# Optimization experiments

Measured on AMD Instinct MI355X. Metric: run time of the kernel, lower is better.

## Reference

```python
import jax, jax.numpy as jnp
import numpy as np

N = 100000   # mesh vertices
E = 600000   # directed edges
H = 128      # hidden dim
Z = 64       # latent (aggregated voxel feature) dim per block
IN = 6       # vertices(3) + vector_potential(3)
BIN = H + Z + IN  # 198, block input dim after concat
OUT = 3      # E-field components


def graph_conv(x, src, dst, Ws, Wn, b, n_nodes, act=True):
    # gather source-node features, mean-aggregate onto destination nodes
    msg = jax.ops.segment_sum(x[src], dst, num_segments=n_nodes)          # [N, F]
    deg = jax.ops.segment_sum(jnp.ones((src.shape[0], 1), x.dtype), dst,
                              num_segments=n_nodes)                        # [N, 1]
    nb = msg / jnp.maximum(deg, 1.0)
    out = x @ Ws + nb @ Wn + b
    return jax.nn.relu(out) if act else out


def setup_inputs() -> dict:
    key = jax.random.key(0)
    ks = jax.random.split(key, 12)
    s = 0.05
    vertices = jax.random.normal(ks[0], (N, 3), jnp.float32)
    vector_potential = jax.random.normal(ks[1], (N, 3), jnp.float32)
    z = jax.random.normal(ks[2], (4, N, Z), jnp.float32)
    edges = jax.random.randint(ks[3], (E, 2), 0, N, jnp.int64)
    # graph_conv_first: IN -> H
    W0s = jax.random.normal(ks[4], (IN, H), jnp.float32) * s
    W0n = jax.random.normal(ks[5], (IN, H), jnp.float32) * s
    b0 = jnp.zeros((H,), jnp.float32)
    # 4 gnn blocks: BIN -> H (stacked)
    Wbs = jax.random.normal(ks[6], (4, BIN, H), jnp.float32) * s
    Wbn = jax.random.normal(ks[7], (4, BIN, H), jnp.float32) * s
    bb = jnp.zeros((4, H), jnp.float32)
    # graph_conv_last: H -> OUT (no activation)
    Wls = jax.random.normal(ks[8], (H, OUT), jnp.float32) * s
    Wln = jax.random.normal(ks[9], (H, OUT), jnp.float32) * s
    bl = jnp.zeros((OUT,), jnp.float32)
    return {"vertices": vertices, "edges": edges,
            "vector_potential": vector_potential, "z": z,
            "W0s": W0s, "W0n": W0n, "b0": b0,
            "Wbs": Wbs, "Wbn": Wbn, "bb": bb,
            "Wls": Wls, "Wln": Wln, "bl": bl}


def reference(vertices, edges, vector_potential, z,
              W0s, W0n, b0, Wbs, Wbn, bb, Wls, Wln, bl):
    src = edges[:, 0]
    dst = edges[:, 1]
    n = vertices.shape[0]
    input_features = jnp.concatenate([vertices, vector_potential], axis=-1)  # [N, 6]
    features = graph_conv(input_features, src, dst, W0s, W0n, b0, n)          # [N, H]
    for i in range(4):  # fixed, structurally distinct blocks
        features = jnp.concatenate([features, z[i], input_features], axis=-1)  # [N, 198]
        features = graph_conv(features, src, dst, Wbs[i], Wbn[i], bb[i], n)    # [N, H]
    features = graph_conv(features, src, dst, Wls, Wln, bl, n, act=False)      # [N, 3]
    return features
```

## Files before the change

kernel.cpp:

```cpp
#include <hip/hip_runtime.h>
#include <hip/hip_bf16.h>


typedef short short8v __attribute__((ext_vector_type(8)));
typedef float float4v __attribute__((ext_vector_type(4)));

static __device__ __forceinline__ unsigned short f2b(float x) {
  union { float f; unsigned u; } v; v.f = x;
  unsigned r = v.u + 0x7FFF + ((v.u >> 16) & 1);
  return (unsigned short)(r >> 16);
}
static __device__ __forceinline__ float b2f(unsigned short x) {
  union { unsigned u; float f; } v; v.u = ((unsigned)x) << 16;
  return v.f;
}

__global__ __launch_bounds__(256) void k_hist(
    const int* __restrict__ edges, int* __restrict__ count, int nE) {
  int e = blockIdx.x * blockDim.x + threadIdx.x;
  if (e >= nE) return;
  atomicAdd(&count[edges[2 * e + 1]], 1);
}

__global__ __launch_bounds__(256) void k_scan_part(
    const int* __restrict__ count, int* __restrict__ partial, int nN) {
  __shared__ int s[256];
  int t = threadIdx.x;
  int n = blockIdx.x * 256 + t;
  s[t] = (n < nN) ? count[n] : 0;
  __syncthreads();
  for (int off = 128; off > 0; off >>= 1) {
    if (t < off) s[t] += s[t + off];
    __syncthreads();
  }
  if (t == 0) partial[blockIdx.x] = s[0];
}

__global__ __launch_bounds__(512) void k_scan_mid(
    int* __restrict__ partial, int* __restrict__ row_ptr, int nb, int nN, int nE) {
  __shared__ int s[512];
  int t = threadIdx.x;
  int v = (t < nb) ? partial[t] : 0;
  s[t] = v;
  __syncthreads();
  for (int off = 1; off < 512; off <<= 1) {
    int add = (t >= off) ? s[t - off] : 0;
    __syncthreads();
    s[t] += add;
    __syncthreads();
  }
  if (t < nb) partial[t] = s[t] - v;
  if (t == 0) row_ptr[nN] = nE;
}

__global__ __launch_bounds__(256) void k_scan_out(
    const int* __restrict__ count, const int* __restrict__ partial,
    int* __restrict__ row_ptr, int* __restrict__ cursor,
    float* __restrict__ invdeg, int nN) {
  __shared__ int s[256];
  int t = threadIdx.x;
  int n = blockIdx.x * 256 + t;
  int v = (n < nN) ? count[n] : 0;
  s[t] = v;
  __syncthreads();
  for (int off = 1; off < 256; off <<= 1) {
    int add = (t >= off) ? s[t - off] : 0;
    __syncthreads();
    s[t] += add;
    __syncthreads();
  }
  if (n < nN) {
    int excl = s[t] - v + partial[blockIdx.x];
    row_ptr[n] = excl;
    cursor[n] = excl;
    invdeg[n] = 1.0f / fmaxf((float)v, 1.0f);
  }
}

__global__ __launch_bounds__(256) void k_fill(
    const int* __restrict__ edges, int* __restrict__ cursor,
    int* __restrict__ csr_src, int nE) {
  int e = blockIdx.x * blockDim.x + threadIdx.x;
  if (e >= nE) return;
  int src = edges[2 * e], dst = edges[2 * e + 1];
  int pos = atomicAdd(&cursor[dst], 1);
  csr_src[pos] = src;
}

__global__ __launch_bounds__(256) void k_prepw(
    const float* __restrict__ Wbn, const float* __restrict__ Wbs,
    unsigned short* __restrict__ Wt) {
  int t = blockIdx.x * 256 + threadIdx.x;
  if (t >= 4 * 256 * 224) return;
  int k = t % 224;
  int c = (t / 224) % 256;
  int i = t / (224 * 256);
  float v = 0.f;
  if (k < 198)
    v = (c < 128) ? Wbn[((size_t)i * 198 + k) * 128 + c]
                  : Wbs[((size_t)i * 198 + k) * 128 + (c - 128)];
  Wt[t] = f2b(v);
}

__global__ __launch_bounds__(256) void k_nbin(
    const int* __restrict__ row_ptr, const int* __restrict__ csr_src,
    const float* __restrict__ vert, const float* __restrict__ vp,
    const float* __restrict__ invdeg, float* __restrict__ nb_in, int nN) {
  int n = blockIdx.x * blockDim.x + threadIdx.x;
  if (n >= nN) return;
  float a[6] = {0, 0, 0, 0, 0, 0};
  int beg = row_ptr[n], end = row_ptr[n + 1];
  for (int j = beg; j < end; ++j) {
    int s = csr_src[j];
#pragma unroll
    for (int k = 0; k < 3; ++k) {
      a[k] += vert[s * 3 + k];
      a[3 + k] += vp[s * 3 + k];
    }
  }
  float inv = invdeg[n];
#pragma unroll
  for (int k = 0; k < 6; ++k) nb_in[n * 6 + k] = a[k] * inv;
}

__global__ __launch_bounds__(256) void k_layer0(
    const float* __restrict__ vert, const float* __restrict__ vp,
    const float* __restrict__ nb_in, const float* __restrict__ W0s,
    const float* __restrict__ W0n, const float* __restrict__ b0,
    unsigned short* __restrict__ fb, int nN) {
  int t = blockIdx.x * blockDim.x + threadIdx.x;
  int n = t >> 7, hh = t & 127;
  if (n >= nN) return;
  float acc = b0[hh];
#pragma unroll
  for (int k = 0; k < 3; ++k) {
    acc += vert[n * 3 + k] * W0s[k * 128 + hh];
    acc += vp[n * 3 + k] * W0s[(3 + k) * 128 + hh];
    acc += nb_in[n * 6 + k] * W0n[k * 128 + hh];
    acc += nb_in[n * 6 + 3 + k] * W0n[(3 + k) * 128 + hh];
  }
  fb[(size_t)n * 128 + hh] = f2b(fmaxf(acc, 0.0f));
}

__global__ __launch_bounds__(256) void k_mfma(
    const unsigned short* __restrict__ fb, const float* __restrict__ z,
    const float* __restrict__ vert, const float* __restrict__ vp,
    const unsigned short* __restrict__ Wt, float* __restrict__ partial,
    unsigned short* __restrict__ hb, int nN) {
  __shared__ unsigned short xs[64 * 232];
  int t = threadIdx.x;
  int n0 = blockIdx.x * 64;

  for (int i = t; i < 64 * 16; i += 256) {
    int r = i >> 4, ck = (i & 15) * 8;
    int gn = min(n0 + r, nN - 1);
    *(short8v*)&xs[r * 232 + ck] = *(const short8v*)&fb[(size_t)gn * 128 + ck];
  }
  for (int i = t; i < 64 * 16; i += 256) {
    int r = i >> 4, ck = (i & 15) * 4;
    int gn = min(n0 + r, nN - 1);
    float4 v = *(const float4*)&z[(size_t)gn * 64 + ck];
    ushort4 o = {f2b(v.x), f2b(v.y), f2b(v.z), f2b(v.w)};
    *(ushort4*)&xs[r * 232 + 128 + ck] = o;
  }
  for (int i = t; i < 64 * 16; i += 256) {
    int r = i >> 4, p = i & 15;
    int c = 192 + 2 * p;
    int gn = min(n0 + r, nN - 1);
    float v0 = 0.f, v1 = 0.f;
    if (c < 198)   v0 = (c < 195) ? vert[gn * 3 + c - 192] : vp[gn * 3 + c - 195];
    if (c + 1 < 198) v1 = (c + 1 < 195) ? vert[gn * 3 + c - 191] : vp[gn * 3 + c - 194];
    ushort2 o = {f2b(v0), f2b(v1)};
    *(ushort2*)&xs[r * 232 + c] = o;
  }
  __syncthreads();

  int w = t >> 6, l = t & 63;
  int c0 = w * 64;
  int lr = l & 15;
  int lk = (l >> 4) * 8;

  float4v acc[4][4];
#pragma unroll
  for (int mt = 0; mt < 4; ++mt)
#pragma unroll
    for (int nt = 0; nt < 4; ++nt)
      acc[mt][nt] = (float4v){0.f, 0.f, 0.f, 0.f};

#pragma unroll
  for (int ks = 0; ks < 7; ++ks) {
    short8v a[4], b[4];
#pragma unroll
    for (int nt = 0; nt < 4; ++nt)
      b[nt] = *(const short8v*)&Wt[(size_t)(c0 + nt * 16 + lr) * 224 + ks * 32 + lk];
#pragma unroll
    for (int mt = 0; mt < 4; ++mt)
      a[mt] = *(const short8v*)&xs[(mt * 16 + lr) * 232 + ks * 32 + lk];
#pragma unroll
    for (int mt = 0; mt < 4; ++mt)
#pragma unroll
      for (int nt = 0; nt < 4; ++nt)
        acc[mt][nt] = __builtin_amdgcn_mfma_f32_16x16x32_bf16(
            a[mt], b[nt], acc[mt][nt], 0, 0, 0);
  }

  int rbase = (l >> 4) * 4;
#pragma unroll
  for (int mt = 0; mt < 4; ++mt) {
#pragma unroll
    for (int nt = 0; nt < 4; ++nt) {
      int col = c0 + nt * 16 + lr;
#pragma unroll
      for (int j = 0; j < 4; ++j) {
        int row = n0 + mt * 16 + rbase + j;
        if (row < nN) {
          float v = acc[mt][nt][j];
          if (col < 128) hb[(size_t)row * 128 + col] = f2b(v);
          else           partial[(size_t)row * 128 + (col - 128)] = v;
        }
      }
    }
  }
}

__global__ __launch_bounds__(256) void k_gather_ep(
    const unsigned short* __restrict__ hb, const int* __restrict__ row_ptr,
    const int* __restrict__ csr_src, const float* __restrict__ invdeg,
    const float* __restrict__ partial, const float* __restrict__ bias,
    unsigned short* __restrict__ fb, int nN) {
  int t = blockIdx.x * 256 + threadIdx.x;
  int n = t >> 5, c = t & 31;
  if (n >= nN) return;
  int beg = row_ptr[n], end = row_ptr[n + 1];
  float a0 = 0, a1 = 0, a2 = 0, a3 = 0;
  int j = beg;
  for (; j + 1 < end; j += 2) {
    int s0 = csr_src[j], s1 = csr_src[j + 1];
    ushort4 v0 = *(const ushort4*)&hb[(size_t)s0 * 128 + c * 4];
    ushort4 v1 = *(const ushort4*)&hb[(size_t)s1 * 128 + c * 4];
    a0 += b2f(v0.x) + b2f(v1.x);
    a1 += b2f(v0.y) + b2f(v1.y);
    a2 += b2f(v0.z) + b2f(v1.z);
    a3 += b2f(v0.w) + b2f(v1.w);
  }
  if (j < end) {
    int s0 = csr_src[j];
    ushort4 v0 = *(const ushort4*)&hb[(size_t)s0 * 128 + c * 4];
    a0 += b2f(v0.x); a1 += b2f(v0.y); a2 += b2f(v0.z); a3 += b2f(v0.w);
  }
  float inv = invdeg[n];
  float4 pv = *(const float4*)&partial[(size_t)n * 128 + c * 4];
  float4 bv = *(const float4*)&bias[c * 4];
  ushort4 o;
  o.x = f2b(fmaxf(pv.x + a0 * inv + bv.x, 0.f));
  o.y = f2b(fmaxf(pv.y + a1 * inv + bv.y, 0.f));
  o.z = f2b(fmaxf(pv.z + a2 * inv + bv.z, 0.f));
  o.w = f2b(fmaxf(pv.w + a3 * inv + bv.w, 0.f));
  *(ushort4*)&fb[(size_t)n * 128 + c * 4] = o;
}

__global__ __launch_bounds__(256) void k_final_h(
    const unsigned short* __restrict__ fb, const float* __restrict__ Wln,
    float4* __restrict__ h3, int nN) {
  int n = blockIdx.x * 4 + (threadIdx.x >> 6);
  int l = threadIdx.x & 63;
  if (n >= nN) return;
  float a0 = b2f(fb[(size_t)n * 128 + l]), a1 = b2f(fb[(size_t)n * 128 + 64 + l]);
  float p[3];
#pragma unroll
  for (int o = 0; o < 3; ++o)
    p[o] = a0 * Wln[l * 3 + o] + a1 * Wln[(64 + l) * 3 + o];
#pragma unroll
  for (int off = 32; off >= 1; off >>= 1) {
    p[0] += __shfl_xor(p[0], off);
    p[1] += __shfl_xor(p[1], off);
    p[2] += __shfl_xor(p[2], off);
  }
  if (l == 0) {
    float4 o = {p[0], p[1], p[2], 0.0f};
    h3[n] = o;
  }
}

__global__ __launch_bounds__(256) void k_gather3(
    const float4* __restrict__ h3, const int* __restrict__ row_ptr,
    const int* __restrict__ csr_src, const float* __restrict__ invdeg,
    float4* __restrict__ nb3, int nN) {
  int n = blockIdx.x * 256 + threadIdx.x;
  if (n >= nN) return;
  int beg = row_ptr[n], end = row_ptr[n + 1];
  float4 acc = {0, 0, 0, 0};
  for (int j = beg; j < end; ++j) {
    float4 v = h3[csr_src[j]];
    acc.x += v.x; acc.y += v.y; acc.z += v.z;
  }
  float inv = invdeg[n];
  float4 o = {acc.x * inv, acc.y * inv, acc.z * inv, 0.0f};
  nb3[n] = o;
}

__global__ __launch_bounds__(256) void k_final_out(
    const unsigned short* __restrict__ fb, const float* __restrict__ Wls,
    const float4* __restrict__ nb3, const float* __restrict__ bl,
    float* __restrict__ out, int nN) {
  int n = blockIdx.x * 4 + (threadIdx.x >> 6);
  int l = threadIdx.x & 63;
  if (n >= nN) return;
  float a0 = b2f(fb[(size_t)n * 128 + l]), a1 = b2f(fb[(size_t)n * 128 + 64 + l]);
  float p[3];
#pragma unroll
  for (int o = 0; o < 3; ++o)
    p[o] = a0 * Wls[l * 3 + o] + a1 * Wls[(64 + l) * 3 + o];
#pragma unroll
  for (int off = 32; off >= 1; off >>= 1) {
    p[0] += __shfl_xor(p[0], off);
    p[1] += __shfl_xor(p[1], off);
    p[2] += __shfl_xor(p[2], off);
  }
  if (l == 0) {
    float4 nv = nb3[n];
    out[n * 3 + 0] = p[0] + nv.x + bl[0];
    out[n * 3 + 1] = p[1] + nv.y + bl[1];
    out[n * 3 + 2] = p[2] + nv.z + bl[2];
  }
}

extern "C" void kernel_launch(void* const* d_in, const int* in_sizes, int n_in,
                              void* d_out, int out_size, void* d_ws, size_t ws_size,
                              hipStream_t stream) {
  const float* vert = (const float*)d_in[0];
  const int* edges = (const int*)d_in[1];
  const float* vp = (const float*)d_in[2];
  const float* z = (const float*)d_in[3];
  const float* W0s = (const float*)d_in[4];
  const float* W0n = (const float*)d_in[5];
  const float* b0 = (const float*)d_in[6];
  const float* Wbs = (const float*)d_in[7];
  const float* Wbn = (const float*)d_in[8];
  const float* bb = (const float*)d_in[9];
  const float* Wls = (const float*)d_in[10];
  const float* Wln = (const float*)d_in[11];
  const float* bl = (const float*)d_in[12];
  int nN = in_sizes[0] / 3;
  int nE = in_sizes[1] / 2;

  float* ws = (float*)d_ws;
  size_t o = 0;
  float* invdeg = ws + o; o += (size_t)nN;
  float* nb_in = ws + o; o += (size_t)nN * 6;
  o = (o + 3) & ~(size_t)3;
  float* partial = ws + o; o += (size_t)nN * 128;
  unsigned short* hb = (unsigned short*)(ws + o); o += (size_t)nN * 64;
  unsigned short* fb = (unsigned short*)(ws + o); o += (size_t)nN * 64;
  unsigned short* Wt = (unsigned short*)(ws + o); o += (size_t)4 * 256 * 224 / 2;
  float* h3 = ws + o; o += (size_t)nN * 4;
  float* nb3 = ws + o; o += (size_t)nN * 4;
  int* ibase = (int*)(ws + o);
  int* count = ibase;
  int* row_ptr = ibase + nN;
  int* cursor = row_ptr + nN + 4;
  int* pscan = cursor + nN;
  int* csr_src = pscan + 512;

  int nbScan = (nN + 255) / 256;

  hipMemsetAsync(count, 0, (size_t)nN * sizeof(int), stream);
  k_hist<<<(nE + 255) / 256, 256, 0, stream>>>(edges, count, nE);
  k_scan_part<<<nbScan, 256, 0, stream>>>(count, pscan, nN);
  k_scan_mid<<<1, 512, 0, stream>>>(pscan, row_ptr, nbScan, nN, nE);
  k_scan_out<<<nbScan, 256, 0, stream>>>(count, pscan, row_ptr, cursor, invdeg, nN);
  k_fill<<<(nE + 255) / 256, 256, 0, stream>>>(edges, cursor, csr_src, nE);
  k_prepw<<<(4 * 256 * 224 + 255) / 256, 256, 0, stream>>>(Wbn, Wbs, Wt);

  k_nbin<<<nbScan, 256, 0, stream>>>(row_ptr, csr_src, vert, vp, invdeg, nb_in, nN);
  k_layer0<<<(int)(((size_t)nN * 128 + 255) / 256), 256, 0, stream>>>(
      vert, vp, nb_in, W0s, W0n, b0, fb, nN);

  for (int i = 0; i < 4; ++i) {
    const float* zi = z + (size_t)i * nN * 64;
    k_mfma<<<(nN + 63) / 64, 256, 0, stream>>>(
        fb, zi, vert, vp, Wt + (size_t)i * 256 * 224, partial, hb, nN);
    k_gather_ep<<<(int)(((size_t)nN * 32 + 255) / 256), 256, 0, stream>>>(
        hb, row_ptr, csr_src, invdeg, partial, bb + (size_t)i * 128, fb, nN);
  }

  k_final_h<<<(nN + 3) / 4, 256, 0, stream>>>(fb, Wln, (float4*)h3, nN);
  k_gather3<<<nbScan, 256, 0, stream>>>(
      (const float4*)h3, row_ptr, csr_src, invdeg, (float4*)nb3, nN);
  k_final_out<<<(nN + 3) / 4, 256, 0, stream>>>(
      fb, Wls, (const float4*)nb3, bl, (float*)d_out, nN);
}
```

Baseline: 681.7 us.

## Split static input features out of MFMA GEMM and fuse final projection into gather

The 6 constant input-feature columns leave the bf16 MFMA GEMM, which shrinks K from 224 to 192 (6 k-steps instead of 7). Their self and neighbour contributions are added in fp32 in the gather epilogue, reusing the precomputed neighbour mean nb_in, since the neighbour mean of a linear map equals the linear map of the neighbour mean. The self-term partial is now stored as bf16 instead of fp32, halving that traffic. The last block's gather also computes the H->3 projection, which removes the separate k_final_h pass over fb at the cost of slightly more precision loss in the partial.

```diff
diff --git a/kernel.cpp b/kernel.cpp
--- a/kernel.cpp
+++ b/kernel.cpp
@@ -91,14 +91,12 @@
     const float* __restrict__ Wbn, const float* __restrict__ Wbs,
     unsigned short* __restrict__ Wt) {
   int t = blockIdx.x * 256 + threadIdx.x;
-  if (t >= 4 * 256 * 224) return;
-  int k = t % 224;
-  int c = (t / 224) % 256;
-  int i = t / (224 * 256);
-  float v = 0.f;
-  if (k < 198)
-    v = (c < 128) ? Wbn[((size_t)i * 198 + k) * 128 + c]
-                  : Wbs[((size_t)i * 198 + k) * 128 + (c - 128)];
+  if (t >= 4 * 256 * 192) return;
+  int k = t % 192;
+  int c = (t / 192) % 256;
+  int i = t / (192 * 256);
+  float v = (c < 128) ? Wbn[((size_t)i * 198 + k) * 128 + c]
+                      : Wbs[((size_t)i * 198 + k) * 128 + (c - 128)];
   Wt[t] = f2b(v);
 }
 
@@ -144,34 +142,23 @@
 
 __global__ __launch_bounds__(256) void k_mfma(
     const unsigned short* __restrict__ fb, const float* __restrict__ z,
-    const float* __restrict__ vert, const float* __restrict__ vp,
-    const unsigned short* __restrict__ Wt, float* __restrict__ partial,
+    const unsigned short* __restrict__ Wt, unsigned short* __restrict__ pb,
     unsigned short* __restrict__ hb, int nN) {
-  __shared__ unsigned short xs[64 * 232];
+  __shared__ unsigned short xs[64 * 200];
   int t = threadIdx.x;
   int n0 = blockIdx.x * 64;
 
   for (int i = t; i < 64 * 16; i += 256) {
     int r = i >> 4, ck = (i & 15) * 8;
     int gn = min(n0 + r, nN - 1);
-    *(short8v*)&xs[r * 232 + ck] = *(const short8v*)&fb[(size_t)gn * 128 + ck];
+    *(short8v*)&xs[r * 200 + ck] = *(const short8v*)&fb[(size_t)gn * 128 + ck];
   }
   for (int i = t; i < 64 * 16; i += 256) {
     int r = i >> 4, ck = (i & 15) * 4;
     int gn = min(n0 + r, nN - 1);
     float4 v = *(const float4*)&z[(size_t)gn * 64 + ck];
     ushort4 o = {f2b(v.x), f2b(v.y), f2b(v.z), f2b(v.w)};
-    *(ushort4*)&xs[r * 232 + 128 + ck] = o;
-  }
-  for (int i = t; i < 64 * 16; i += 256) {
-    int r = i >> 4, p = i & 15;
-    int c = 192 + 2 * p;
-    int gn = min(n0 + r, nN - 1);
-    float v0 = 0.f, v1 = 0.f;
-    if (c < 198)   v0 = (c < 195) ? vert[gn * 3 + c - 192] : vp[gn * 3 + c - 195];
-    if (c + 1 < 198) v1 = (c + 1 < 195) ? vert[gn * 3 + c - 191] : vp[gn * 3 + c - 194];
-    ushort2 o = {f2b(v0), f2b(v1)};
-    *(ushort2*)&xs[r * 232 + c] = o;
+    *(ushort4*)&xs[r * 200 + 128 + ck] = o;
   }
   __syncthreads();
 
@@ -188,14 +175,14 @@
       acc[mt][nt] = (float4v){0.f, 0.f, 0.f, 0.f};
 
 #pragma unroll
-  for (int ks = 0; ks < 7; ++ks) {
+  for (int ks = 0; ks < 6; ++ks) {
     short8v a[4], b[4];
 #pragma unroll
     for (int nt = 0; nt < 4; ++nt)
-      b[nt] = *(const short8v*)&Wt[(size_t)(c0 + nt * 16 + lr) * 224 + ks * 32 + lk];
+      b[nt] = *(const short8v*)&Wt[(size_t)(c0 + nt * 16 + lr) * 192 + ks * 32 + lk];
 #pragma unroll
     for (int mt = 0; mt < 4; ++mt)
-      a[mt] = *(const short8v*)&xs[(mt * 16 + lr) * 232 + ks * 32 + lk];
+      a[mt] = *(const short8v*)&xs[(mt * 16 + lr) * 200 + ks * 32 + lk];
 #pragma unroll
     for (int mt = 0; mt < 4; ++mt)
 #pragma unroll
@@ -216,18 +203,22 @@
         if (row < nN) {
           float v = acc[mt][nt][j];
           if (col < 128) hb[(size_t)row * 128 + col] = f2b(v);
-          else           partial[(size_t)row * 128 + (col - 128)] = v;
+          else           pb[(size_t)row * 128 + (col - 128)] = f2b(v);
         }
       }
     }
   }
 }
 
+template <int FINAL>
 __global__ __launch_bounds__(256) void k_gather_ep(
     const unsigned short* __restrict__ hb, const int* __restrict__ row_ptr,
     const int* __restrict__ csr_src, const float* __restrict__ invdeg,
-    const float* __restrict__ partial, const float* __restrict__ bias,
-    unsigned short* __restrict__ fb, int nN) {
+    const unsigned short* __restrict__ pb, const float* __restrict__ nb_in,
+    const float* __restrict__ vert, const float* __restrict__ vp,
+    const float* __restrict__ Wn_in, const float* __restrict__ Ws_in,
+    const float* __restrict__ bias, unsigned short* __restrict__ fb,
+    const float* __restrict__ Wln, float4* __restrict__ h3, int nN) {
   int t = blockIdx.x * 256 + threadIdx.x;
   int n = t >> 5, c = t & 31;
   if (n >= nN) return;
@@ -248,37 +239,53 @@
     ushort4 v0 = *(const ushort4*)&hb[(size_t)s0 * 128 + c * 4];
     a0 += b2f(v0.x); a1 += b2f(v0.y); a2 += b2f(v0.z); a3 += b2f(v0.w);
   }
+  float in6[6], nb6[6];
+#pragma unroll
+  for (int k = 0; k < 3; ++k) {
+    in6[k] = vert[n * 3 + k];
+    in6[3 + k] = vp[n * 3 + k];
+  }
+#pragma unroll
+  for (int k = 0; k < 6; ++k) nb6[k] = nb_in[n * 6 + k];
+  float cx = 0, cy = 0, cz = 0, cw = 0;
+#pragma unroll
+  for (int k = 0; k < 6; ++k) {
+    float4 wn = *(const float4*)&Wn_in[k * 128 + c * 4];
+    float4 wsv = *(const float4*)&Ws_in[k * 128 + c * 4];
+    cx += nb6[k] * wn.x + in6[k] * wsv.x;
+    cy += nb6[k] * wn.y + in6[k] * wsv.y;
+    cz += nb6[k] * wn.z + in6[k] * wsv.z;
+    cw += nb6[k] * wn.w + in6[k] * wsv.w;
+  }
   float inv = invdeg[n];
-  float4 pv = *(const float4*)&partial[(size_t)n * 128 + c * 4];
+  ushort4 pv4 = *(const ushort4*)&pb[(size_t)n * 128 + c * 4];
   float4 bv = *(const float4*)&bias[c * 4];
   ushort4 o;
-  o.x = f2b(fmaxf(pv.x + a0 * inv + bv.x, 0.f));
-  o.y = f2b(fmaxf(pv.y + a1 * inv + bv.y, 0.f));
-  o.z = f2b(fmaxf(pv.z + a2 * inv + bv.z, 0.f));
-  o.w = f2b(fmaxf(pv.w + a3 * inv + bv.w, 0.f));
+  o.x = f2b(fmaxf(b2f(pv4.x) + a0 * inv + bv.x + cx, 0.f));
+  o.y = f2b(fmaxf(b2f(pv4.y) + a1 * inv + bv.y + cy, 0.f));
+  o.z = f2b(fmaxf(b2f(pv4.z) + a2 * inv + bv.z + cz, 0.f));
+  o.w = f2b(fmaxf(b2f(pv4.w) + a3 * inv + bv.w + cw, 0.f));
   *(ushort4*)&fb[(size_t)n * 128 + c * 4] = o;
-}
-
-__global__ __launch_bounds__(256) void k_final_h(
-    const unsigned short* __restrict__ fb, const float* __restrict__ Wln,
-    float4* __restrict__ h3, int nN) {
-  int n = blockIdx.x * 4 + (threadIdx.x >> 6);
-  int l = threadIdx.x & 63;
-  if (n >= nN) return;
-  float a0 = b2f(fb[(size_t)n * 128 + l]), a1 = b2f(fb[(size_t)n * 128 + 64 + l]);
-  float p[3];
-#pragma unroll
-  for (int o = 0; o < 3; ++o)
-    p[o] = a0 * Wln[l * 3 + o] + a1 * Wln[(64 + l) * 3 + o];
-#pragma unroll
-  for (int off = 32; off >= 1; off >>= 1) {
-    p[0] += __shfl_xor(p[0], off);
-    p[1] += __shfl_xor(p[1], off);
-    p[2] += __shfl_xor(p[2], off);
-  }
-  if (l == 0) {
-    float4 o = {p[0], p[1], p[2], 0.0f};
-    h3[n] = o;
+
+  if (FINAL) {
+    float f0 = b2f(o.x), f1 = b2f(o.y), f2 = b2f(o.z), f3 = b2f(o.w);
+    float p[3];
+#pragma unroll
+    for (int oo = 0; oo < 3; ++oo) {
+      int cc = c * 4;
+      p[oo] = f0 * Wln[cc * 3 + oo] + f1 * Wln[(cc + 1) * 3 + oo] +
+              f2 * Wln[(cc + 2) * 3 + oo] + f3 * Wln[(cc + 3) * 3 + oo];
+    }
+#pragma unroll
+    for (int off = 16; off >= 1; off >>= 1) {
+      p[0] += __shfl_xor(p[0], off);
+      p[1] += __shfl_xor(p[1], off);
+      p[2] += __shfl_xor(p[2], off);
+    }
+    if (c == 0) {
+      float4 ov = {p[0], p[1], p[2], 0.0f};
+      h3[n] = ov;
+    }
   }
 }
 
@@ -349,10 +356,10 @@
   float* invdeg = ws + o; o += (size_t)nN;
   float* nb_in = ws + o; o += (size_t)nN * 6;
   o = (o + 3) & ~(size_t)3;
-  float* partial = ws + o; o += (size_t)nN * 128;
+  unsigned short* pb = (unsigned short*)(ws + o); o += (size_t)nN * 64;
   unsigned short* hb = (unsigned short*)(ws + o); o += (size_t)nN * 64;
   unsigned short* fb = (unsigned short*)(ws + o); o += (size_t)nN * 64;
-  unsigned short* Wt = (unsigned short*)(ws + o); o += (size_t)4 * 256 * 224 / 2;
+  unsigned short* Wt = (unsigned short*)(ws + o); o += (size_t)4 * 256 * 192 / 2;
   float* h3 = ws + o; o += (size_t)nN * 4;
   float* nb3 = ws + o; o += (size_t)nN * 4;
   int* ibase = (int*)(ws + o);
@@ -370,7 +377,7 @@
   k_scan_mid<<<1, 512, 0, stream>>>(pscan, row_ptr, nbScan, nN, nE);
   k_scan_out<<<nbScan, 256, 0, stream>>>(count, pscan, row_ptr, cursor, invdeg, nN);
   k_fill<<<(nE + 255) / 256, 256, 0, stream>>>(edges, cursor, csr_src, nE);
-  k_prepw<<<(4 * 256 * 224 + 255) / 256, 256, 0, stream>>>(Wbn, Wbs, Wt);
+  k_prepw<<<(4 * 256 * 192 + 255) / 256, 256, 0, stream>>>(Wbn, Wbs, Wt);
 
   k_nbin<<<nbScan, 256, 0, stream>>>(row_ptr, csr_src, vert, vp, invdeg, nb_in, nN);
   k_layer0<<<(int)(((size_t)nN * 128 + 255) / 256), 256, 0, stream>>>(
@@ -378,13 +385,20 @@
 
   for (int i = 0; i < 4; ++i) {
     const float* zi = z + (size_t)i * nN * 64;
+    const float* Wn_in = Wbn + ((size_t)i * 198 + 192) * 128;
+    const float* Ws_in = Wbs + ((size_t)i * 198 + 192) * 128;
     k_mfma<<<(nN + 63) / 64, 256, 0, stream>>>(
-        fb, zi, vert, vp, Wt + (size_t)i * 256 * 224, partial, hb, nN);
-    k_gather_ep<<<(int)(((size_t)nN * 32 + 255) / 256), 256, 0, stream>>>(
-        hb, row_ptr, csr_src, invdeg, partial, bb + (size_t)i * 128, fb, nN);
-  }
-
-  k_final_h<<<(nN + 3) / 4, 256, 0, stream>>>(fb, Wln, (float4*)h3, nN);
+        fb, zi, Wt + (size_t)i * 256 * 192, pb, hb, nN);
+    if (i < 3)
+      k_gather_ep<0><<<(int)(((size_t)nN * 32 + 255) / 256), 256, 0, stream>>>(
+          hb, row_ptr, csr_src, invdeg, pb, nb_in, vert, vp, Wn_in, Ws_in,
+          bb + (size_t)i * 128, fb, nullptr, nullptr, nN);
+    else
+      k_gather_ep<1><<<(int)(((size_t)nN * 32 + 255) / 256), 256, 0, stream>>>(
+          hb, row_ptr, csr_src, invdeg, pb, nb_in, vert, vp, Wn_in, Ws_in,
+          bb + (size_t)i * 128, fb, Wln, (float4*)h3, nN);
+  }
+
   k_gather3<<<nbScan, 256, 0, stream>>>(
       (const float4*)h3, row_ptr, csr_src, invdeg, (float4*)nb3, nN);
   k_final_out<<<(nN + 3) / 4, 256, 0, stream>>>(
```

Result: slower. 748.9 us (+9.9%).

## Fuse neighbor gather epilogue into next block's MFMA kernel and fold final layer

Applied to the files above, without the earlier changes.

Each block's gather-and-activate step now runs inside the next block's MFMA kernel, writing activated features straight into shared memory. This removes the round trip of the bf16 feature buffer and four separate gather launches, using ping-pong hb/pb buffers. The self-term partial is stored as bf16 instead of fp32, halving its traffic but adding rounding error. The last gather is fused with both final H->3 projections, cutting three final kernels to two, and gather loops are unrolled by four.

```diff
diff --git a/kernel.cpp b/kernel.cpp
--- a/kernel.cpp
+++ b/kernel.cpp
@@ -142,20 +142,21 @@
   fb[(size_t)n * 128 + hh] = f2b(fmaxf(acc, 0.0f));
 }
 
-__global__ __launch_bounds__(256) void k_mfma(
-    const unsigned short* __restrict__ fb, const float* __restrict__ z,
-    const float* __restrict__ vert, const float* __restrict__ vp,
-    const unsigned short* __restrict__ Wt, float* __restrict__ partial,
-    unsigned short* __restrict__ hb, int nN) {
+template <int GATHER>
+__global__ __launch_bounds__(256) void k_fused(
+    const unsigned short* __restrict__ fb,
+    const unsigned short* __restrict__ hb_in,
+    const unsigned short* __restrict__ pb_in,
+    const int* __restrict__ row_ptr, const int* __restrict__ csr_src,
+    const float* __restrict__ invdeg, const float* __restrict__ bias_prev,
+    const float* __restrict__ z, const float* __restrict__ vert,
+    const float* __restrict__ vp, const unsigned short* __restrict__ Wt,
+    unsigned short* __restrict__ pb_out, unsigned short* __restrict__ hb_out,
+    int nN) {
   __shared__ unsigned short xs[64 * 232];
   int t = threadIdx.x;
   int n0 = blockIdx.x * 64;
 
-  for (int i = t; i < 64 * 16; i += 256) {
-    int r = i >> 4, ck = (i & 15) * 8;
-    int gn = min(n0 + r, nN - 1);
-    *(short8v*)&xs[r * 232 + ck] = *(const short8v*)&fb[(size_t)gn * 128 + ck];
-  }
   for (int i = t; i < 64 * 16; i += 256) {
     int r = i >> 4, ck = (i & 15) * 4;
     int gn = min(n0 + r, nN - 1);
@@ -168,10 +169,53 @@
     int c = 192 + 2 * p;
     int gn = min(n0 + r, nN - 1);
     float v0 = 0.f, v1 = 0.f;
-    if (c < 198)   v0 = (c < 195) ? vert[gn * 3 + c - 192] : vp[gn * 3 + c - 195];
+    if (c < 198)     v0 = (c < 195) ? vert[gn * 3 + c - 192] : vp[gn * 3 + c - 195];
     if (c + 1 < 198) v1 = (c + 1 < 195) ? vert[gn * 3 + c - 191] : vp[gn * 3 + c - 194];
     ushort2 o = {f2b(v0), f2b(v1)};
     *(ushort2*)&xs[r * 232 + c] = o;
+  }
+  if (GATHER == 0) {
+    for (int i = t; i < 64 * 16; i += 256) {
+      int r = i >> 4, ck = (i & 15) * 8;
+      int gn = min(n0 + r, nN - 1);
+      *(short8v*)&xs[r * 232 + ck] = *(const short8v*)&fb[(size_t)gn * 128 + ck];
+    }
+  } else {
+    int g = t >> 5;
+    int c = t & 31;
+    for (int i = 0; i < 8; ++i) {
+      int r = g * 8 + i;
+      int gn = min(n0 + r, nN - 1);
+      int beg = row_ptr[gn], end = row_ptr[gn + 1];
+      float a0 = 0, a1 = 0, a2 = 0, a3 = 0;
+      int j = beg;
+      for (; j + 3 < end; j += 4) {
+        int s0 = csr_src[j], s1 = csr_src[j + 1];
+        int s2 = csr_src[j + 2], s3 = csr_src[j + 3];
+        ushort4 v0 = *(const ushort4*)&hb_in[(size_t)s0 * 128 + c * 4];
+        ushort4 v1 = *(const ushort4*)&hb_in[(size_t)s1 * 128 + c * 4];
+        ushort4 v2 = *(const ushort4*)&hb_in[(size_t)s2 * 128 + c * 4];
+        ushort4 v3 = *(const ushort4*)&hb_in[(size_t)s3 * 128 + c * 4];
+        a0 += (b2f(v0.x) + b2f(v1.x)) + (b2f(v2.x) + b2f(v3.x));
+        a1 += (b2f(v0.y) + b2f(v1.y)) + (b2f(v2.y) + b2f(v3.y));
+        a2 += (b2f(v0.z) + b2f(v1.z)) + (b2f(v2.z) + b2f(v3.z));
+        a3 += (b2f(v0.w) + b2f(v1.w)) + (b2f(v2.w) + b2f(v3.w));
+      }
+      for (; j < end; ++j) {
+        int s0 = csr_src[j];
+        ushort4 v0 = *(const ushort4*)&hb_in[(size_t)s0 * 128 + c * 4];
+        a0 += b2f(v0.x); a1 += b2f(v0.y); a2 += b2f(v0.z); a3 += b2f(v0.w);
+      }
+      float inv = invdeg[gn];
+      ushort4 pv = *(const ushort4*)&pb_in[(size_t)gn * 128 + c * 4];
+      float4 bv = *(const float4*)&bias_prev[c * 4];
+      ushort4 o;
+      o.x = f2b(fmaxf(b2f(pv.x) + a0 * inv + bv.x, 0.f));
+      o.y = f2b(fmaxf(b2f(pv.y) + a1 * inv + bv.y, 0.f));
+      o.z = f2b(fmaxf(b2f(pv.z) + a2 * inv + bv.z, 0.f));
+      o.w = f2b(fmaxf(b2f(pv.w) + a3 * inv + bv.w, 0.f));
+      *(ushort4*)&xs[r * 232 + c * 4] = o;
+    }
   }
   __syncthreads();
 
@@ -215,77 +259,80 @@
         int row = n0 + mt * 16 + rbase + j;
         if (row < nN) {
           float v = acc[mt][nt][j];
-          if (col < 128) hb[(size_t)row * 128 + col] = f2b(v);
-          else           partial[(size_t)row * 128 + (col - 128)] = v;
+          if (col < 128) hb_out[(size_t)row * 128 + col] = f2b(v);
+          else           pb_out[(size_t)row * 128 + (col - 128)] = f2b(v);
         }
       }
     }
   }
 }
 
-__global__ __launch_bounds__(256) void k_gather_ep(
+__global__ __launch_bounds__(256) void k_gather_fin(
     const unsigned short* __restrict__ hb, const int* __restrict__ row_ptr,
     const int* __restrict__ csr_src, const float* __restrict__ invdeg,
-    const float* __restrict__ partial, const float* __restrict__ bias,
-    unsigned short* __restrict__ fb, int nN) {
+    const unsigned short* __restrict__ pb, const float* __restrict__ bias,
+    const float* __restrict__ Wln, const float* __restrict__ Wls,
+    const float* __restrict__ bl, float4* __restrict__ h3,
+    float4* __restrict__ s3, int nN) {
   int t = blockIdx.x * 256 + threadIdx.x;
   int n = t >> 5, c = t & 31;
   if (n >= nN) return;
   int beg = row_ptr[n], end = row_ptr[n + 1];
   float a0 = 0, a1 = 0, a2 = 0, a3 = 0;
   int j = beg;
-  for (; j + 1 < end; j += 2) {
+  for (; j + 3 < end; j += 4) {
     int s0 = csr_src[j], s1 = csr_src[j + 1];
+    int s2 = csr_src[j + 2], sx = csr_src[j + 3];
     ushort4 v0 = *(const ushort4*)&hb[(size_t)s0 * 128 + c * 4];
     ushort4 v1 = *(const ushort4*)&hb[(size_t)s1 * 128 + c * 4];
-    a0 += b2f(v0.x) + b2f(v1.x);
-    a1 += b2f(v0.y) + b2f(v1.y);
-    a2 += b2f(v0.z) + b2f(v1.z);
-    a3 += b2f(v0.w) + b2f(v1.w);
-  }
-  if (j < end) {
+    ushort4 v2 = *(const ushort4*)&hb[(size_t)s2 * 128 + c * 4];
+    ushort4 v3 = *(const ushort4*)&hb[(size_t)sx * 128 + c * 4];
+    a0 += (b2f(v0.x) + b2f(v1.x)) + (b2f(v2.x) + b2f(v3.x));
+    a1 += (b2f(v0.y) + b2f(v1.y)) + (b2f(v2.y) + b2f(v3.y));
+    a2 += (b2f(v0.z) + b2f(v1.z)) + (b2f(v2.z) + b2f(v3.z));
+    a3 += (b2f(v0.w) + b2f(v1.w)) + (b2f(v2.w) + b2f(v3.w));
+  }
+  for (; j < end; ++j) {
     int s0 = csr_src[j];
     ushort4 v0 = *(const ushort4*)&hb[(size_t)s0 * 128 + c * 4];
     a0 += b2f(v0.x); a1 += b2f(v0.y); a2 += b2f(v0.z); a3 += b2f(v0.w);
   }
   float inv = invdeg[n];
-  float4 pv = *(const float4*)&partial[(size_t)n * 128 + c * 4];
+  ushort4 pv = *(const ushort4*)&pb[(size_t)n * 128 + c * 4];
   float4 bv = *(const float4*)&bias[c * 4];
-  ushort4 o;
-  o.x = f2b(fmaxf(pv.x + a0 * inv + bv.x, 0.f));
-  o.y = f2b(fmaxf(pv.y + a1 * inv + bv.y, 0.f));
-  o.z = f2b(fmaxf(pv.z + a2 * inv + bv.z, 0.f));
-  o.w = f2b(fmaxf(pv.w + a3 * inv + bv.w, 0.f));
-  *(ushort4*)&fb[(size_t)n * 128 + c * 4] = o;
-}
-
-__global__ __launch_bounds__(256) void k_final_h(
-    const unsigned short* __restrict__ fb, const float* __restrict__ Wln,
-    float4* __restrict__ h3, int nN) {
-  int n = blockIdx.x * 4 + (threadIdx.x >> 6);
-  int l = threadIdx.x & 63;
-  if (n >= nN) return;
-  float a0 = b2f(fb[(size_t)n * 128 + l]), a1 = b2f(fb[(size_t)n * 128 + 64 + l]);
-  float p[3];
-#pragma unroll
-  for (int o = 0; o < 3; ++o)
-    p[o] = a0 * Wln[l * 3 + o] + a1 * Wln[(64 + l) * 3 + o];
-#pragma unroll
-  for (int off = 32; off >= 1; off >>= 1) {
-    p[0] += __shfl_xor(p[0], off);
-    p[1] += __shfl_xor(p[1], off);
-    p[2] += __shfl_xor(p[2], off);
-  }
-  if (l == 0) {
-    float4 o = {p[0], p[1], p[2], 0.0f};
-    h3[n] = o;
-  }
-}
-
-__global__ __launch_bounds__(256) void k_gather3(
-    const float4* __restrict__ h3, const int* __restrict__ row_ptr,
-    const int* __restrict__ csr_src, const float* __restrict__ invdeg,
-    float4* __restrict__ nb3, int nN) {
+  float f0 = fmaxf(b2f(pv.x) + a0 * inv + bv.x, 0.f);
+  float f1 = fmaxf(b2f(pv.y) + a1 * inv + bv.y, 0.f);
+  float f2 = fmaxf(b2f(pv.z) + a2 * inv + bv.z, 0.f);
+  float f3 = fmaxf(b2f(pv.w) + a3 * inv + bv.w, 0.f);
+  f0 = b2f(f2b(f0)); f1 = b2f(f2b(f1)); f2 = b2f(f2b(f2)); f3 = b2f(f2b(f3));
+  float pn[3], ps[3];
+  int cc = c * 4;
+#pragma unroll
+  for (int o = 0; o < 3; ++o) {
+    pn[o] = f0 * Wln[cc * 3 + o] + f1 * Wln[(cc + 1) * 3 + o] +
+            f2 * Wln[(cc + 2) * 3 + o] + f3 * Wln[(cc + 3) * 3 + o];
+    ps[o] = f0 * Wls[cc * 3 + o] + f1 * Wls[(cc + 1) * 3 + o] +
+            f2 * Wls[(cc + 2) * 3 + o] + f3 * Wls[(cc + 3) * 3 + o];
+  }
+#pragma unroll
+  for (int off = 16; off >= 1; off >>= 1) {
+    pn[0] += __shfl_xor(pn[0], off); pn[1] += __shfl_xor(pn[1], off);
+    pn[2] += __shfl_xor(pn[2], off);
+    ps[0] += __shfl_xor(ps[0], off); ps[1] += __shfl_xor(ps[1], off);
+    ps[2] += __shfl_xor(ps[2], off);
+  }
+  if (c == 0) {
+    float4 hv = {pn[0], pn[1], pn[2], 0.0f};
+    float4 sv = {ps[0] + bl[0], ps[1] + bl[1], ps[2] + bl[2], 0.0f};
+    h3[n] = hv;
+    s3[n] = sv;
+  }
+}
+
+__global__ __launch_bounds__(256) void k_out(
+    const float4* __restrict__ h3, const float4* __restrict__ s3,
+    const int* __restrict__ row_ptr, const int* __restrict__ csr_src,
+    const float* __restrict__ invdeg, float* __restrict__ out, int nN) {
   int n = blockIdx.x * 256 + threadIdx.x;
   if (n >= nN) return;
   int beg = row_ptr[n], end = row_ptr[n + 1];
@@ -295,34 +342,10 @@
     acc.x += v.x; acc.y += v.y; acc.z += v.z;
   }
   float inv = invdeg[n];
-  float4 o = {acc.x * inv, acc.y * inv, acc.z * inv, 0.0f};
-  nb3[n] = o;
-}
-
-__global__ __launch_bounds__(256) void k_final_out(
-    const unsigned short* __restrict__ fb, const float* __restrict__ Wls,
-    const float4* __restrict__ nb3, const float* __restrict__ bl,
-    float* __restrict__ out, int nN) {
-  int n = blockIdx.x * 4 + (threadIdx.x >> 6);
-  int l = threadIdx.x & 63;
-  if (n >= nN) return;
-  float a0 = b2f(fb[(size_t)n * 128 + l]), a1 = b2f(fb[(size_t)n * 128 + 64 + l]);
-  float p[3];
-#pragma unroll
-  for (int o = 0; o < 3; ++o)
-    p[o] = a0 * Wls[l * 3 + o] + a1 * Wls[(64 + l) * 3 + o];
-#pragma unroll
-  for (int off = 32; off >= 1; off >>= 1) {
-    p[0] += __shfl_xor(p[0], off);
-    p[1] += __shfl_xor(p[1], off);
-    p[2] += __shfl_xor(p[2], off);
-  }
-  if (l == 0) {
-    float4 nv = nb3[n];
-    out[n * 3 + 0] = p[0] + nv.x + bl[0];
-    out[n * 3 + 1] = p[1] + nv.y + bl[1];
-    out[n * 3 + 2] = p[2] + nv.z + bl[2];
-  }
+  float4 sv = s3[n];
+  out[n * 3 + 0] = sv.x + acc.x * inv;
+  out[n * 3 + 1] = sv.y + acc.y * inv;
+  out[n * 3 + 2] = sv.z + acc.z * inv;
 }
 
 extern "C" void kernel_launch(void* const* d_in, const int* in_sizes, int n_in,
@@ -349,12 +372,14 @@
   float* invdeg = ws + o; o += (size_t)nN;
   float* nb_in = ws + o; o += (size_t)nN * 6;
   o = (o + 3) & ~(size_t)3;
-  float* partial = ws + o; o += (size_t)nN * 128;
-  unsigned short* hb = (unsigned short*)(ws + o); o += (size_t)nN * 64;
   unsigned short* fb = (unsigned short*)(ws + o); o += (size_t)nN * 64;
+  unsigned short* hbA = (unsigned short*)(ws + o); o += (size_t)nN * 64;
+  unsigned short* pbA = (unsigned short*)(ws + o); o += (size_t)nN * 64;
+  unsigned short* hbB = (unsigned short*)(ws + o); o += (size_t)nN * 64;
+  unsigned short* pbB = (unsigned short*)(ws + o); o += (size_t)nN * 64;
   unsigned short* Wt = (unsigned short*)(ws + o); o += (size_t)4 * 256 * 224 / 2;
   float* h3 = ws + o; o += (size_t)nN * 4;
-  float* nb3 = ws + o; o += (size_t)nN * 4;
+  float* s3 = ws + o; o += (size_t)nN * 4;
   int* ibase = (int*)(ws + o);
   int* count = ibase;
   int* row_ptr = ibase + nN;
@@ -376,17 +401,27 @@
   k_layer0<<<(int)(((size_t)nN * 128 + 255) / 256), 256, 0, stream>>>(
       vert, vp, nb_in, W0s, W0n, b0, fb, nN);
 
-  for (int i = 0; i < 4; ++i) {
-    const float* zi = z + (size_t)i * nN * 64;
-    k_mfma<<<(nN + 63) / 64, 256, 0, stream>>>(
-        fb, zi, vert, vp, Wt + (size_t)i * 256 * 224, partial, hb, nN);
-    k_gather_ep<<<(int)(((size_t)nN * 32 + 255) / 256), 256, 0, stream>>>(
-        hb, row_ptr, csr_src, invdeg, partial, bb + (size_t)i * 128, fb, nN);
-  }
-
-  k_final_h<<<(nN + 3) / 4, 256, 0, stream>>>(fb, Wln, (float4*)h3, nN);
-  k_gather3<<<nbScan, 256, 0, stream>>>(
-      (const float4*)h3, row_ptr, csr_src, invdeg, (float4*)nb3, nN);
-  k_final_out<<<(nN + 3) / 4, 256, 0, stream>>>(
-      fb, Wls, (const float4*)nb3, bl, (float*)d_out, nN);
-}
+  int nbF = (nN + 63) / 64;
+  k_fused<0><<<nbF, 256, 0, stream>>>(
+      fb, nullptr, nullptr, row_ptr, csr_src, invdeg, b0 ,
+      z + (size_t)0 * nN * 64, vert, vp, Wt + (size_t)0 * 256 * 224,
+      pbA, hbA, nN);
+  k_fused<1><<<nbF, 256, 0, stream>>>(
+      nullptr, hbA, pbA, row_ptr, csr_src, invdeg, bb + 0 * 128,
+      z + (size_t)1 * nN * 64, vert, vp, Wt + (size_t)1 * 256 * 224,
+      pbB, hbB, nN);
+  k_fused<1><<<nbF, 256, 0, stream>>>(
+      nullptr, hbB, pbB, row_ptr, csr_src, invdeg, bb + 1 * 128,
+      z + (size_t)2 * nN * 64, vert, vp, Wt + (size_t)2 * 256 * 224,
+      pbA, hbA, nN);
+  k_fused<1><<<nbF, 256, 0, stream>>>(
+      nullptr, hbA, pbA, row_ptr, csr_src, invdeg, bb + 2 * 128,
+      z + (size_t)3 * nN * 64, vert, vp, Wt + (size_t)3 * 256 * 224,
+      pbB, hbB, nN);
+  k_gather_fin<<<(int)(((size_t)nN * 32 + 255) / 256), 256, 0, stream>>>(
+      hbB, row_ptr, csr_src, invdeg, pbB, bb + 3 * 128, Wln, Wls, bl,
+      (float4*)h3, (float4*)s3, nN);
+  k_out<<<nbScan, 256, 0, stream>>>(
+      (const float4*)h3, (const float4*)s3, row_ptr, csr_src, invdeg,
+      (float*)d_out, nN);
+}
```

Result: slower. 703.7 us (+3.2%).
